# Kernel tuning notes

Hardware: AMD Instinct MI355X
Metric: run time of the kernel (lower is better)

The kernel has to match this reference:

```python
import jax, jax.numpy as jnp
import numpy as np

FEATURE_IN = 4096
FEATURE_OUT = 4096
R = 16
ALPHA = 32.0


def setup_inputs() -> dict:
    key = jax.random.key(0)
    k_x, k_w, k_b, k_a = jax.random.split(key, 4)
    x = jax.random.normal(k_x, (4, 2048, FEATURE_IN), dtype=jnp.float32)
    # base linear (torch nn.Linear): weight [out, in], bias [out]
    bound = 1.0 / np.sqrt(FEATURE_IN)
    w = jax.random.uniform(k_w, (FEATURE_OUT, FEATURE_IN), dtype=jnp.float32, minval=-bound, maxval=bound)
    b = jax.random.uniform(k_b, (FEATURE_OUT,), dtype=jnp.float32, minval=-bound, maxval=bound)
    # lora_a: kaiming uniform over [feature_in, r]; lora_b: zeros -> use small randn so grads are nontrivial? No: faithful init is zeros, but zeros makes LoRA path trivially zero. Use kaiming for a, small random for b to exercise the math.
    gain = np.sqrt(2.0 / (1.0 + 5.0 ** 2))  # kaiming_uniform default a=sqrt(5)
    bound_a = gain * np.sqrt(3.0 / FEATURE_IN)
    lora_a = jax.random.uniform(k_a, (FEATURE_IN, R), dtype=jnp.float32, minval=-bound_a, maxval=bound_a)
    lora_b = jax.random.normal(jax.random.fold_in(key, 7), (R, FEATURE_OUT), dtype=jnp.float32) * 0.01
    return {"x": x, "w": w, "b": b, "lora_a": lora_a, "lora_b": lora_b}


def reference(x, w, b, lora_a, lora_b):
    # base linear: x @ W^T + b
    output1 = jnp.einsum('bsi,oi->bso', x, w) + b
    # faithful to source: materialize (A @ B) [feature_in, feature_out] first,
    # then x @ (A@B), scaled by alpha/r
    ab = jnp.matmul(lora_a, lora_b)  # [feature_in, feature_out]
    output2 = jnp.matmul(x, ab) * (ALPHA / R)
    return output2 + output1
```

## Files before the change

### kernel.cpp

```cpp
#include <hip/hip_runtime.h>
#include <cstdint>
#include <cstddef>

#define FEATURE_IN 4096
#define FEATURE_OUT 4096
#define RNK 16

typedef __bf16 bf16x8_t __attribute__((ext_vector_type(8)));
typedef float f32x4_t __attribute__((ext_vector_type(4)));

#define FW_KB 128
#define FW_NB 32
#define NCVT 16384
#define NFUSE 4096

__global__ __launch_bounds__(256) void prep_kernel(const float* __restrict__ x,
                                                   uint16_t* __restrict__ xb,
                                                   const float* __restrict__ w,
                                                   const float* __restrict__ la,
                                                   const float* __restrict__ lb,
                                                   uint16_t* __restrict__ wf) {
    __shared__ float las[FW_KB * RNK];
    __shared__ float lbs[RNK * FW_NB];

    const int tid = threadIdx.x;

    if (blockIdx.x < NCVT) {
        int i = blockIdx.x * 256 + tid;
        const float4* xp = (const float4*)x;
        float4 v0 = xp[2 * i];
        float4 v1 = xp[2 * i + 1];
        bf16x8_t o;
        o[0] = (__bf16)v0.x; o[1] = (__bf16)v0.y; o[2] = (__bf16)v0.z; o[3] = (__bf16)v0.w;
        o[4] = (__bf16)v1.x; o[5] = (__bf16)v1.y; o[6] = (__bf16)v1.z; o[7] = (__bf16)v1.w;
        ((bf16x8_t*)xb)[i] = o;
        return;
    }

    const int bid = blockIdx.x - NCVT;
    const int kb = (bid & 31) * FW_KB;
    const int nb = (bid >> 5) * FW_NB;

    {
        const float4* src = (const float4*)(la + (size_t)kb * RNK);
        float4* dst = (float4*)las;
        dst[tid] = src[tid];
        dst[tid + 256] = src[tid + 256];
    }
#pragma unroll
    for (int f = tid; f < RNK * FW_NB; f += 256) {
        int r = f >> 5;
        int nl = f & 31;
        lbs[r * FW_NB + nl] = lb[(size_t)r * FEATURE_OUT + nb + nl];
    }
    __syncthreads();

    const int nl = tid >> 3;
    const int kq = tid & 7;

    f32x4_t bcol[4];
#pragma unroll
    for (int r4 = 0; r4 < 4; ++r4) {
        f32x4_t v;
#pragma unroll
        for (int j = 0; j < 4; ++j) v[j] = lbs[(r4 * 4 + j) * FW_NB + nl];
        bcol[r4] = v;
    }

    const f32x4_t* las4 = (const f32x4_t*)las;
    const float* wrow = w + (size_t)(nb + nl) * FEATURE_IN + kb + kq * 16;
    uint16_t* wfrow = wf + (size_t)(nb + nl) * FEATURE_IN + kb + kq * 16;

#pragma unroll
    for (int h = 0; h < 2; ++h) {
        float4 wv0 = ((const float4*)wrow)[h * 2 + 0];
        float4 wv1 = ((const float4*)wrow)[h * 2 + 1];
        float wfv[8] = {wv0.x, wv0.y, wv0.z, wv0.w, wv1.x, wv1.y, wv1.z, wv1.w};
        bf16x8_t o;
#pragma unroll
        for (int j = 0; j < 8; ++j) {
            const int k = kq * 16 + h * 8 + j;
            float s = 0.f;
#pragma unroll
            for (int rr = 0; rr < 4; ++rr) {
                const int r4 = (rr + kq) & 3;
                f32x4_t av = las4[k * 4 + r4];
                f32x4_t bv = bcol[r4];
                s += av[0] * bv[0] + av[1] * bv[1] + av[2] * bv[2] + av[3] * bv[3];
            }
            o[j] = (__bf16)(wfv[j] + 2.f * s);
        }
        ((bf16x8_t*)wfrow)[h] = o;
    }
}

#define BM 128
#define BN 128
#define BK 32

__global__ __launch_bounds__(256) void gemm_bt(const uint16_t* __restrict__ Au,
                                               const uint16_t* __restrict__ Bu,
                                               const float* __restrict__ bias,
                                               float* __restrict__ C,
                                               int M, int N, int K) {
    __shared__ __bf16 As[BM * BK];
    __shared__ __bf16 Bs[BN * BK];

    const __bf16* A = (const __bf16*)Au;
    const __bf16* B = (const __bf16*)Bu;

    const int wv    = threadIdx.x >> 6;
    const int lane  = threadIdx.x & 63;
    const int waveM = wv >> 1;
    const int waveN = wv & 1;
    const int m0 = blockIdx.y * BM;
    const int n0 = blockIdx.x * BN;

    const int rowInCall = lane >> 2;
    const int kOff      = (lane & 3) * 8;

    const int l15  = lane & 15;
    const int quad = lane >> 4;
    const int aoff = l15 * BK + quad * 8;

    const int c0 = wv * 2, c1 = wv * 2 + 1;
    const __bf16* ga0 = A + (size_t)(m0 + c0 * 16 + rowInCall) * K + kOff;
    const __bf16* ga1 = A + (size_t)(m0 + c1 * 16 + rowInCall) * K + kOff;
    const __bf16* gb0 = B + (size_t)(n0 + c0 * 16 + rowInCall) * K + kOff;
    const __bf16* gb1 = B + (size_t)(n0 + c1 * 16 + rowInCall) * K + kOff;
    auto* asDst0 = (__attribute__((address_space(3))) void*)&As[c0 * 512];
    auto* asDst1 = (__attribute__((address_space(3))) void*)&As[c1 * 512];
    auto* bsDst0 = (__attribute__((address_space(3))) void*)&Bs[c0 * 512];
    auto* bsDst1 = (__attribute__((address_space(3))) void*)&Bs[c1 * 512];

    f32x4_t acc[4][4];
#pragma unroll
    for (int mi = 0; mi < 4; ++mi)
#pragma unroll
        for (int ni = 0; ni < 4; ++ni)
            acc[mi][ni] = (f32x4_t)0.f;

    for (int k0 = 0; k0 < K; k0 += BK) {
        __syncthreads();
        __builtin_amdgcn_global_load_lds((const __attribute__((address_space(1))) void*)ga0,
                                         asDst0, 16, 0, 0);
        __builtin_amdgcn_global_load_lds((const __attribute__((address_space(1))) void*)ga1,
                                         asDst1, 16, 0, 0);
        __builtin_amdgcn_global_load_lds((const __attribute__((address_space(1))) void*)gb0,
                                         bsDst0, 16, 0, 0);
        __builtin_amdgcn_global_load_lds((const __attribute__((address_space(1))) void*)gb1,
                                         bsDst1, 16, 0, 0);
        ga0 += BK; ga1 += BK; gb0 += BK; gb1 += BK;
        __syncthreads();

        bf16x8_t af[4], bfr[4];
#pragma unroll
        for (int mi = 0; mi < 4; ++mi)
            af[mi] = *(const bf16x8_t*)&As[(waveM * 64 + mi * 16) * BK + aoff];
#pragma unroll
        for (int ni = 0; ni < 4; ++ni)
            bfr[ni] = *(const bf16x8_t*)&Bs[(waveN * 64 + ni * 16) * BK + aoff];

#pragma unroll
        for (int mi = 0; mi < 4; ++mi)
#pragma unroll
            for (int ni = 0; ni < 4; ++ni)
                acc[mi][ni] = __builtin_amdgcn_mfma_f32_16x16x32_bf16(af[mi], bfr[ni],
                                                                      acc[mi][ni], 0, 0, 0);
    }

#pragma unroll
    for (int ni = 0; ni < 4; ++ni) {
        const int col = n0 + waveN * 64 + ni * 16 + l15;
        const float bv = bias[col];
#pragma unroll
        for (int mi = 0; mi < 4; ++mi) {
            const int row = m0 + waveM * 64 + mi * 16 + quad * 4;
            float* op = C + (size_t)row * N + col;
#pragma unroll
            for (int j = 0; j < 4; ++j)
                op[(size_t)j * N] = acc[mi][ni][j] + bv;
        }
    }
}

extern "C" void kernel_launch(void* const* d_in, const int* in_sizes, int n_in,
                              void* d_out, int out_size, void* d_ws, size_t ws_size,
                              hipStream_t stream) {
    const float* x  = (const float*)d_in[0];
    const float* w  = (const float*)d_in[1];
    const float* b  = (const float*)d_in[2];
    const float* la = (const float*)d_in[3];
    const float* lb = (const float*)d_in[4];
    float* out = (float*)d_out;

    const int M = in_sizes[0] / FEATURE_IN;
    const int K = FEATURE_IN;
    const int N = FEATURE_OUT;

    uint16_t* xb = (uint16_t*)d_ws;
    uint16_t* wf = (uint16_t*)((char*)d_ws + (size_t)M * K * 2);

    prep_kernel<<<NCVT + NFUSE, 256, 0, stream>>>(x, xb, w, la, lb, wf);

    {
        dim3 grid(N / BN, M / BM);
        gemm_bt<<<grid, 256, 0, stream>>>(xb, wf, b, out, M, N, K);
    }
}
```

Baseline: 629.9 us.

## Replace GEMM with 256x256 double-buffered pipelined MFMA kernel with swizzled LDS

After: 518.1 us. 1.22x faster.

```diff
diff --git a/kernel.cpp b/kernel.cpp
--- a/kernel.cpp
+++ b/kernel.cpp
@@ -7,6 +7,7 @@
 #define RNK 16
 
 typedef __bf16 bf16x8_t __attribute__((ext_vector_type(8)));
+typedef __bf16 bf16x4_t __attribute__((ext_vector_type(4)));
 typedef float f32x4_t __attribute__((ext_vector_type(4)));
 
 #define FW_KB 128
@@ -26,14 +27,15 @@
     const int tid = threadIdx.x;
 
     if (blockIdx.x < NCVT) {
-        int i = blockIdx.x * 256 + tid;
+        const int base = blockIdx.x * 512;
         const float4* xp = (const float4*)x;
-        float4 v0 = xp[2 * i];
-        float4 v1 = xp[2 * i + 1];
-        bf16x8_t o;
-        o[0] = (__bf16)v0.x; o[1] = (__bf16)v0.y; o[2] = (__bf16)v0.z; o[3] = (__bf16)v0.w;
-        o[4] = (__bf16)v1.x; o[5] = (__bf16)v1.y; o[6] = (__bf16)v1.z; o[7] = (__bf16)v1.w;
-        ((bf16x8_t*)xb)[i] = o;
+        float4 v0 = xp[base + tid];
+        float4 v1 = xp[base + 256 + tid];
+        bf16x4_t o0, o1;
+        o0[0] = (__bf16)v0.x; o0[1] = (__bf16)v0.y; o0[2] = (__bf16)v0.z; o0[3] = (__bf16)v0.w;
+        o1[0] = (__bf16)v1.x; o1[1] = (__bf16)v1.y; o1[2] = (__bf16)v1.z; o1[3] = (__bf16)v1.w;
+        ((bf16x4_t*)xb)[base + tid] = o0;
+        ((bf16x4_t*)xb)[base + 256 + tid] = o1;
         return;
     }
 
@@ -94,88 +96,167 @@
     }
 }
 
-#define BM 128
-#define BN 128
-#define BK 32
-
-__global__ __launch_bounds__(256) void gemm_bt(const uint16_t* __restrict__ Au,
-                                               const uint16_t* __restrict__ Bu,
-                                               const float* __restrict__ bias,
-                                               float* __restrict__ C,
-                                               int M, int N, int K) {
-    __shared__ __bf16 As[BM * BK];
-    __shared__ __bf16 Bs[BN * BK];
+#define BM 256
+#define BN 256
+#define BK 64
+#define NT (FEATURE_IN / BK)
+
+#define ABASE(P, KS) ((P) * 65536 + (KS) * 16384)
+#define BBASE(P, KS) ((P) * 65536 + 32768 + (KS) * 16384)
+
+#define READ_A(G, P, KS) do { _Pragma("unroll")                                          \
+    for (int _mi = 0; _mi < 4; ++_mi)                                                    \
+        a[_mi] = *(const bf16x8_t*)(lds + ABASE(P, KS) + aoff[(G) * 4 + _mi]); } while (0)
+
+#define READ_B(P, KS) do { _Pragma("unroll")                                             \
+    for (int _ni = 0; _ni < 4; ++_ni)                                                    \
+        b[_ni] = *(const bf16x8_t*)(lds + BBASE(P, KS) + boff[_ni]); } while (0)
+
+#define MFMA_G(G) do { _Pragma("unroll")                                                 \
+    for (int _mi = 0; _mi < 4; ++_mi) { _Pragma("unroll")                                \
+        for (int _ni = 0; _ni < 4; ++_ni)                                                \
+            acc[(G) * 4 + _mi][_ni] = __builtin_amdgcn_mfma_f32_16x16x32_bf16(           \
+                a[_mi], b[_ni], acc[(G) * 4 + _mi][_ni], 0, 0, 0); } } while (0)
+
+#define STAGE_A(PN, KS) do {                                                             \
+    __builtin_amdgcn_global_load_lds(                                                    \
+        (const __attribute__((address_space(1))) void*)(pA0 + (KS) * 32),                \
+        (__attribute__((address_space(3))) void*)(lds + ABASE(PN, KS) + wv * 1024),      \
+        16, 0, 0);                                                                       \
+    __builtin_amdgcn_global_load_lds(                                                    \
+        (const __attribute__((address_space(1))) void*)(pA1 + (KS) * 32),                \
+        (__attribute__((address_space(3))) void*)(lds + ABASE(PN, KS) + 8192 + wv * 1024),\
+        16, 0, 0); } while (0)
+
+#define STAGE_B(PN, KS) do {                                                             \
+    __builtin_amdgcn_global_load_lds(                                                    \
+        (const __attribute__((address_space(1))) void*)(pB0 + (KS) * 32),                \
+        (__attribute__((address_space(3))) void*)(lds + BBASE(PN, KS) + wv * 1024),      \
+        16, 0, 0);                                                                       \
+    __builtin_amdgcn_global_load_lds(                                                    \
+        (const __attribute__((address_space(1))) void*)(pB1 + (KS) * 32),                \
+        (__attribute__((address_space(3))) void*)(lds + BBASE(PN, KS) + 8192 + wv * 1024),\
+        16, 0, 0); } while (0)
+
+#define PBAR() __builtin_amdgcn_s_barrier()
+#define PRIO1 __builtin_amdgcn_s_setprio(1)
+#define PRIO0 __builtin_amdgcn_s_setprio(0)
+#define VMCNT(n) asm volatile("s_waitcnt vmcnt(" #n ")" ::: "memory")
+
+#define TILE_BODY(P, PN)                                                                 \
+                                                                            \
+    READ_A(0, P, 0); READ_B(P, 0);                                                       \
+    STAGE_A(PN, 0);                                                                      \
+    PBAR();                                                                              \
+    PRIO1; MFMA_G(0); PRIO0;                                                             \
+    PBAR();                                                                              \
+                                                                            \
+    READ_A(1, P, 0);                                                                     \
+    STAGE_B(PN, 0);                                                                      \
+    PBAR();                                                                              \
+    PRIO1; MFMA_G(1); PRIO0;                                                             \
+    VMCNT(4);       \
+    PBAR();                                                                              \
+                                                                            \
+    READ_A(0, P, 1); READ_B(P, 1);                                                       \
+    STAGE_A(PN, 1);                                                                      \
+    PBAR();                                                                              \
+    PRIO1; MFMA_G(0); PRIO0;                                                             \
+    PBAR();                                                                              \
+                                                                            \
+    READ_A(1, P, 1);                                                                     \
+    STAGE_B(PN, 1);                                                                      \
+    PBAR();                                                                              \
+    PRIO1; MFMA_G(1); PRIO0;                                                             \
+    VMCNT(4);                                      \
+    PBAR();                                                                              \
+    pA0 += BK; pA1 += BK; pB0 += BK; pB1 += BK;
+
+__global__ __launch_bounds__(512, 2) void gemm256(const uint16_t* __restrict__ Au,
+                                                  const uint16_t* __restrict__ Bu,
+                                                  const float* __restrict__ bias,
+                                                  float* __restrict__ C,
+                                                  int M, int N, int K) {
+    __shared__ __align__(16) char lds[131072];
 
     const __bf16* A = (const __bf16*)Au;
     const __bf16* B = (const __bf16*)Bu;
 
-    const int wv    = threadIdx.x >> 6;
-    const int lane  = threadIdx.x & 63;
-    const int waveM = wv >> 1;
-    const int waveN = wv & 1;
-    const int m0 = blockIdx.y * BM;
-    const int n0 = blockIdx.x * BN;
-
-    const int rowInCall = lane >> 2;
-    const int kOff      = (lane & 3) * 8;
-
-    const int l15  = lane & 15;
-    const int quad = lane >> 4;
-    const int aoff = l15 * BK + quad * 8;
-
-    const int c0 = wv * 2, c1 = wv * 2 + 1;
-    const __bf16* ga0 = A + (size_t)(m0 + c0 * 16 + rowInCall) * K + kOff;
-    const __bf16* ga1 = A + (size_t)(m0 + c1 * 16 + rowInCall) * K + kOff;
-    const __bf16* gb0 = B + (size_t)(n0 + c0 * 16 + rowInCall) * K + kOff;
-    const __bf16* gb1 = B + (size_t)(n0 + c1 * 16 + rowInCall) * K + kOff;
-    auto* asDst0 = (__attribute__((address_space(3))) void*)&As[c0 * 512];
-    auto* asDst1 = (__attribute__((address_space(3))) void*)&As[c1 * 512];
-    auto* bsDst0 = (__attribute__((address_space(3))) void*)&Bs[c0 * 512];
-    auto* bsDst1 = (__attribute__((address_space(3))) void*)&Bs[c1 * 512];
-
-    f32x4_t acc[4][4];
-#pragma unroll
-    for (int mi = 0; mi < 4; ++mi)
+    const int tid  = threadIdx.x;
+    const int wv   = tid >> 6;
+    const int lane = tid & 63;
+    const int waveM = wv >> 2;
+    const int waveN = wv & 3;
+    const int l15 = lane & 15;
+    const int q   = lane >> 4;
+
+    const int nbx = N / BN;
+    const int nwg = nbx * (M / BM);
+    const int bidlin = blockIdx.y * nbx + blockIdx.x;
+    const int swz = (bidlin & 7) * (nwg >> 3) + (bidlin >> 3);
+    const int by = swz / nbx;
+    const int bx = swz - by * nbx;
+    const int m0 = by * BM;
+    const int n0 = bx * BN;
+
+    const int srow = tid >> 2;
+    const int sq   = ((tid & 3) - (srow >> 1)) & 3;
+    const __bf16* pA0 = A + (size_t)(m0 + srow) * K + sq * 8;
+    const __bf16* pA1 = pA0 + (size_t)128 * K;
+    const __bf16* pB0 = B + (size_t)(n0 + srow) * K + sq * 8;
+    const __bf16* pB1 = pB0 + (size_t)128 * K;
+
+    int aoff[8], boff[4];
+#pragma unroll
+    for (int mi = 0; mi < 8; ++mi) {
+        int row = waveM * 128 + mi * 16 + l15;
+        aoff[mi] = row * 64 + (((row >> 1) + q) & 3) * 16;
+    }
+#pragma unroll
+    for (int ni = 0; ni < 4; ++ni) {
+        int row = waveN * 64 + ni * 16 + l15;
+        boff[ni] = row * 64 + (((row >> 1) + q) & 3) * 16;
+    }
+
+    f32x4_t acc[8][4];
+#pragma unroll
+    for (int mi = 0; mi < 8; ++mi)
 #pragma unroll
         for (int ni = 0; ni < 4; ++ni)
             acc[mi][ni] = (f32x4_t)0.f;
 
-    for (int k0 = 0; k0 < K; k0 += BK) {
-        __syncthreads();
-        __builtin_amdgcn_global_load_lds((const __attribute__((address_space(1))) void*)ga0,
-                                         asDst0, 16, 0, 0);
-        __builtin_amdgcn_global_load_lds((const __attribute__((address_space(1))) void*)ga1,
-                                         asDst1, 16, 0, 0);
-        __builtin_amdgcn_global_load_lds((const __attribute__((address_space(1))) void*)gb0,
-                                         bsDst0, 16, 0, 0);
-        __builtin_amdgcn_global_load_lds((const __attribute__((address_space(1))) void*)gb1,
-                                         bsDst1, 16, 0, 0);
-        ga0 += BK; ga1 += BK; gb0 += BK; gb1 += BK;
-        __syncthreads();
-
-        bf16x8_t af[4], bfr[4];
-#pragma unroll
-        for (int mi = 0; mi < 4; ++mi)
-            af[mi] = *(const bf16x8_t*)&As[(waveM * 64 + mi * 16) * BK + aoff];
-#pragma unroll
-        for (int ni = 0; ni < 4; ++ni)
-            bfr[ni] = *(const bf16x8_t*)&Bs[(waveN * 64 + ni * 16) * BK + aoff];
-
-#pragma unroll
-        for (int mi = 0; mi < 4; ++mi)
-#pragma unroll
-            for (int ni = 0; ni < 4; ++ni)
-                acc[mi][ni] = __builtin_amdgcn_mfma_f32_16x16x32_bf16(af[mi], bfr[ni],
-                                                                      acc[mi][ni], 0, 0, 0);
-    }
+    bf16x8_t a[4], b[4];
+
+    STAGE_A(0, 0); STAGE_B(0, 0); STAGE_A(0, 1); STAGE_B(0, 1);
+    pA0 += BK; pA1 += BK; pB0 += BK; pB1 += BK;
+    VMCNT(4);
+    PBAR();
+
+#pragma unroll 1
+    for (int i = 0; i < (NT - 2) / 2; ++i) {
+        TILE_BODY(0, 1)
+        TILE_BODY(1, 0)
+    }
+    TILE_BODY(0, 1)
+
+    READ_A(0, 1, 0); READ_B(1, 0);
+    PRIO1; MFMA_G(0); PRIO0;
+    READ_A(1, 1, 0);
+    PRIO1; MFMA_G(1); PRIO0;
+    VMCNT(0);
+    PBAR();
+    READ_A(0, 1, 1); READ_B(1, 1);
+    PRIO1; MFMA_G(0); PRIO0;
+    READ_A(1, 1, 1);
+    PRIO1; MFMA_G(1); PRIO0;
 
 #pragma unroll
     for (int ni = 0; ni < 4; ++ni) {
         const int col = n0 + waveN * 64 + ni * 16 + l15;
         const float bv = bias[col];
 #pragma unroll
-        for (int mi = 0; mi < 4; ++mi) {
-            const int row = m0 + waveM * 64 + mi * 16 + quad * 4;
+        for (int mi = 0; mi < 8; ++mi) {
+            const int row = m0 + waveM * 128 + mi * 16 + q * 4;
             float* op = C + (size_t)row * N + col;
 #pragma unroll
             for (int j = 0; j < 4; ++j)
@@ -205,6 +286,6 @@
 
     {
         dim3 grid(N / BN, M / BM);
-        gemm_bt<<<grid, 256, 0, stream>>>(xb, wf, b, out, M, N, K);
+        gemm256<<<grid, 512, 0, stream>>>(xb, wf, b, out, M, N, K);
     }
 }
```
